# Kernel tuning notes

Measured on AMD Instinct MI355X. Metric: run time of the kernel, lower is better.

The kernel has to match this reference:

```python
import jax, jax.numpy as jnp
import numpy as np

HIDDEN_SIZE = 512  # H * d = 8 * 64


def setup_inputs() -> dict:
    key = jax.random.key(0)
    kq, kk, kv = jax.random.split(key, 3)
    B, H, S, d = 2, 8, 4096, 64
    Q = jax.random.normal(kq, (B, H, S, d), dtype=jnp.float32)
    K = jax.random.normal(kk, (B, H, d, S), dtype=jnp.float32)  # pre-transposed, as the torch module expects
    V = jax.random.normal(kv, (B, H, S, d), dtype=jnp.float32)
    return {"Q": Q, "K": K, "V": V}


def reference(Q, K, V):
    B, H, S, d = Q.shape
    scale = 1.0 / np.sqrt(HIDDEN_SIZE).astype(np.float32)
    # e: [B,H,S,S] -- full score matrix, as in the original
    e = jnp.einsum('bhsd,bhdt->bhst', Q, K) * scale
    # FAITHFUL quirk: nn.Softmax(dim=1) normalizes over the HEAD axis, not keys
    a = jax.nn.softmax(e, axis=1)
    o = jnp.einsum('bhst,bhtd->bhsd', a, V)
    # torch .view(B, S, hidden): raw contiguous reshape of [B,H,S,d]
    return o.reshape(B, S, HIDDEN_SIZE)
```

## Files before the change

kernel.cpp:

```cpp
#include <hip/hip_runtime.h>
#include <hip/hip_fp16.h>

#define S_LEN 4096
#define NHEAD 8
#define HEADD 64
#define BM 64
#define BN 32
#define TSPLIT 4
#define NTILE (S_LEN / (TSPLIT * BN))
#define O_ELEMS (2 * NHEAD * S_LEN * HEADD)
#define SCALE 0.04419417382415922f
#define EAPAD 36

#define KT_BYTES (2ull * NHEAD * S_LEN * HEADD * 2)
#define VT_OFF   KT_BYTES
#define PART_OFF (2 * KT_BYTES)
#define WS_FULL  (PART_OFF + (size_t)TSPLIT * O_ELEMS * 4)

typedef __attribute__((ext_vector_type(8))) short   short8;
typedef __attribute__((ext_vector_type(4))) float   float4v;
typedef __attribute__((ext_vector_type(4))) unsigned short ushort4v;

__device__ __forceinline__ unsigned short f2bf(float f) {
  unsigned int u = __float_as_uint(f);
  u += 0x7FFFu + ((u >> 16) & 1u);
  return (unsigned short)(u >> 16);
}

__global__ __launch_bounds__(256)
void prepass_cvt(const float* __restrict__ K, const float* __restrict__ V,
                 unsigned short* __restrict__ Kt, unsigned short* __restrict__ Vt) {
  __shared__ __align__(16) unsigned short lds[64][72];
  const int tid = threadIdx.x;
  const int isV = blockIdx.x >> 10;
  const int idx = blockIdx.x & 1023;
  const int bh  = idx >> 6;
  const int t0  = (idx & 63) << 6;
  if (!isV) {
    const float* in = K + (size_t)bh * HEADD * S_LEN;
#pragma unroll
    for (int j = 0; j < 16; ++j) {
      int li = j * 256 + tid;
      int k = li >> 6, t = li & 63;
      lds[t][k] = f2bf(in[(size_t)k * S_LEN + t0 + t]);
    }
    __syncthreads();
    unsigned short* out = Kt + (size_t)bh * S_LEN * HEADD;
    int t = tid >> 2, k0 = (tid & 3) << 4;
    *(short8*)(out + (size_t)(t0 + t) * HEADD + k0)     = *(const short8*)&lds[t][k0];
    *(short8*)(out + (size_t)(t0 + t) * HEADD + k0 + 8) = *(const short8*)&lds[t][k0 + 8];
  } else {
    const float* in = V + (size_t)bh * S_LEN * HEADD;
#pragma unroll
    for (int j = 0; j < 16; ++j) {
      int li = j * 256 + tid;
      int t = li >> 6, d = li & 63;
      lds[d][t] = f2bf(in[(size_t)(t0 + t) * HEADD + d]);
    }
    __syncthreads();
    unsigned short* out = Vt + (size_t)bh * HEADD * S_LEN;
    int d = tid >> 2, c0 = (tid & 3) << 4;
    *(short8*)(out + (size_t)d * S_LEN + t0 + c0)     = *(const short8*)&lds[d][c0];
    *(short8*)(out + (size_t)d * S_LEN + t0 + c0 + 8) = *(const short8*)&lds[d][c0 + 8];
  }
}

__global__ __launch_bounds__(512, 4)
void attn_main(const float* __restrict__ Q, const unsigned short* __restrict__ Kt,
               const unsigned short* __restrict__ Vt, float* __restrict__ outp,
               int atomic_mode) {
  __shared__ __align__(16) unsigned short EA[2][NHEAD][BM][EAPAD];

  const int tid  = threadIdx.x;
  const int h    = tid >> 6;
  const int lane = tid & 63;
  const int quad = lane >> 4;
  const int l15  = lane & 15;
  const int combo = blockIdx.x & 7;
  const int b  = combo >> 2;
  const int tc = combo & 3;
  const int s0 = (blockIdx.x >> 3) * BM;

  const float* Qg = Q + (size_t)(b * NHEAD + h) * S_LEN * HEADD;
  const unsigned short* Kth = Kt + (size_t)(b * NHEAD + h) * S_LEN * HEADD;
  const unsigned short* Vth = Vt + (size_t)(b * NHEAD + h) * HEADD * S_LEN;

  short8 qf[4][2];
#pragma unroll
  for (int ss = 0; ss < 4; ++ss)
#pragma unroll
    for (int kk = 0; kk < 2; ++kk) {
      const float* p = Qg + (size_t)(s0 + ss * 16 + l15) * HEADD + kk * 32 + quad * 8;
      float4v a0 = *(const float4v*)p;
      float4v a1 = *(const float4v*)(p + 4);
      short8 f;
      f[0] = (short)f2bf(a0[0]); f[1] = (short)f2bf(a0[1]);
      f[2] = (short)f2bf(a0[2]); f[3] = (short)f2bf(a0[3]);
      f[4] = (short)f2bf(a1[0]); f[5] = (short)f2bf(a1[1]);
      f[6] = (short)f2bf(a1[2]); f[7] = (short)f2bf(a1[3]);
      qf[ss][kk] = f;
    }

  float4v acc[4][4];
#pragma unroll
  for (int ss = 0; ss < 4; ++ss)
#pragma unroll
    for (int ds = 0; ds < 4; ++ds)
      acc[ss][ds] = (float4v){0.f, 0.f, 0.f, 0.f};

  const int s_sm = tid >> 3;
  const int t4   = (tid & 7) * 4;

  for (int it = 0; it < NTILE; ++it) {
    const int t0 = tc * (S_LEN / TSPLIT) + it * BN;
    const int p  = it & 1;

    short8 kf[2][2];
#pragma unroll
    for (int ts = 0; ts < 2; ++ts)
#pragma unroll
      for (int kk = 0; kk < 2; ++kk)
        kf[ts][kk] = *(const short8*)(Kth + (size_t)(t0 + ts * 16 + l15) * HEADD + kk * 32 + quad * 8);

#pragma unroll
    for (int ts = 0; ts < 2; ++ts)
#pragma unroll
      for (int ss = 0; ss < 4; ++ss) {
        float4v e = (float4v){0.f, 0.f, 0.f, 0.f};
        e = __builtin_amdgcn_mfma_f32_16x16x32_bf16(qf[ss][0], kf[ts][0], e, 0, 0, 0);
        e = __builtin_amdgcn_mfma_f32_16x16x32_bf16(qf[ss][1], kf[ts][1], e, 0, 0, 0);
#pragma unroll
        for (int r = 0; r < 4; ++r)
          EA[p][h][ss * 16 + quad * 4 + r][ts * 16 + l15] =
              __half_as_ushort(__float2half(e[r] * SCALE));
      }
    __syncthreads();

    {
      float ev[8][4];
#pragma unroll
      for (int hh = 0; hh < 8; ++hh) {
        ushort4v u = *(const ushort4v*)&EA[p][hh][s_sm][t4];
#pragma unroll
        for (int c = 0; c < 4; ++c) ev[hh][c] = __half2float(__ushort_as_half(u[c]));
      }
#pragma unroll
      for (int c = 0; c < 4; ++c) {
        float sum = 0.f;
#pragma unroll
        for (int hh = 0; hh < 8; ++hh) { float x = __expf(ev[hh][c]); ev[hh][c] = x; sum += x; }
        float inv = __builtin_amdgcn_rcpf(sum);
#pragma unroll
        for (int hh = 0; hh < 8; ++hh) ev[hh][c] *= inv;
      }
#pragma unroll
      for (int hh = 0; hh < 8; ++hh) {
        ushort4v u;
#pragma unroll
        for (int c = 0; c < 4; ++c) u[c] = f2bf(ev[hh][c]);
        *(ushort4v*)&EA[p][hh][s_sm][t4] = u;
      }
    }
    __syncthreads();

    short8 af[4], vf[4];
#pragma unroll
    for (int ss = 0; ss < 4; ++ss) {
      union { short8 s8; ushort4v u4[2]; } t;
      t.u4[0] = *(const ushort4v*)&EA[p][h][ss * 16 + l15][quad * 8];
      t.u4[1] = *(const ushort4v*)&EA[p][h][ss * 16 + l15][quad * 8 + 4];
      af[ss] = t.s8;
    }
#pragma unroll
    for (int ds = 0; ds < 4; ++ds)
      vf[ds] = *(const short8*)(Vth + (size_t)(ds * 16 + l15) * S_LEN + t0 + quad * 8);
#pragma unroll
    for (int ss = 0; ss < 4; ++ss)
#pragma unroll
      for (int ds = 0; ds < 4; ++ds)
        acc[ss][ds] = __builtin_amdgcn_mfma_f32_16x16x32_bf16(af[ss], vf[ds], acc[ss][ds], 0, 0, 0);
  }

  float* Og = outp + (atomic_mode ? (size_t)0 : (size_t)tc * O_ELEMS) +
              (size_t)(b * NHEAD + h) * S_LEN * HEADD;
#pragma unroll
  for (int ss = 0; ss < 4; ++ss)
#pragma unroll
    for (int ds = 0; ds < 4; ++ds)
#pragma unroll
      for (int r = 0; r < 4; ++r) {
        size_t off = (size_t)(s0 + ss * 16 + quad * 4 + r) * HEADD + ds * 16 + l15;
        if (atomic_mode) atomicAdd(&Og[off], acc[ss][ds][r]);
        else             Og[off] = acc[ss][ds][r];
      }
}

__global__ __launch_bounds__(256)
void reduce_partials(const float* __restrict__ part, float* __restrict__ out) {
  const int n4 = O_ELEMS / 4;
  const float4v* p = (const float4v*)part;
  float4v* o = (float4v*)out;
  for (int i = blockIdx.x * 256 + threadIdx.x; i < n4; i += gridDim.x * 256) {
    float4v v = p[i] + p[n4 + i] + p[2 * n4 + i] + p[3 * n4 + i];
    o[i] = v;
  }
}

__global__ __launch_bounds__(512, 2)
void attn_fallback(const float* __restrict__ Qg0, const float* __restrict__ Kg0,
                   const float* __restrict__ Vg0, float* __restrict__ Og0) {
  __shared__ __align__(16) unsigned short Klds[NHEAD][BN][72];
  __shared__ __align__(16) unsigned short Vlds[NHEAD][HEADD][40];
  __shared__ __align__(16) unsigned short EA2[NHEAD][BM][40];
  const int tid = threadIdx.x, h = tid >> 6, lane = tid & 63, quad = lane >> 4, l15 = lane & 15;
  const int b = blockIdx.x >> 6, s0 = (blockIdx.x & 63) * BM;
  const float* Qg = Qg0 + ((size_t)(b * NHEAD + h)) * S_LEN * HEADD;
  const float* Kg = Kg0 + ((size_t)(b * NHEAD + h)) * HEADD * S_LEN;
  const float* Vg = Vg0 + ((size_t)(b * NHEAD + h)) * S_LEN * HEADD;
  float* Og = Og0 + ((size_t)(b * NHEAD + h)) * S_LEN * HEADD;
  short8 qf[4][2];
#pragma unroll
  for (int ss = 0; ss < 4; ++ss)
#pragma unroll
    for (int kk = 0; kk < 2; ++kk) {
      const float* p = Qg + (size_t)(s0 + ss * 16 + l15) * HEADD + kk * 32 + quad * 8;
      float4v a0 = *(const float4v*)p; float4v a1 = *(const float4v*)(p + 4);
      short8 f;
      f[0] = (short)f2bf(a0[0]); f[1] = (short)f2bf(a0[1]); f[2] = (short)f2bf(a0[2]); f[3] = (short)f2bf(a0[3]);
      f[4] = (short)f2bf(a1[0]); f[5] = (short)f2bf(a1[1]); f[6] = (short)f2bf(a1[2]); f[7] = (short)f2bf(a1[3]);
      qf[ss][kk] = f;
    }
  float4v acc[4][4];
#pragma unroll
  for (int ss = 0; ss < 4; ++ss)
#pragma unroll
    for (int ds = 0; ds < 4; ++ds) acc[ss][ds] = (float4v){0.f, 0.f, 0.f, 0.f};
  const int koct = lane >> 3, kt4 = (lane & 7) * 4, vdq = lane & 15, vtg = lane >> 4;
  const int s_sm = tid >> 3, t4_sm = (tid & 7) * 4;
  for (int it = 0; it < S_LEN / BN; ++it) {
    const int t0 = it * BN;
    {
      float buf[8][4];
#pragma unroll
      for (int j = 0; j < 8; ++j) {
        float4v v = *(const float4v*)(Kg + (size_t)(koct * 8 + j) * S_LEN + t0 + kt4);
        buf[j][0] = v[0]; buf[j][1] = v[1]; buf[j][2] = v[2]; buf[j][3] = v[3];
      }
#pragma unroll
      for (int c = 0; c < 4; ++c) {
        short8 f;
#pragma unroll
        for (int j = 0; j < 8; ++j) f[j] = (short)f2bf(buf[j][c]);
        *(short8*)&Klds[h][kt4 + c][koct * 8] = f;
      }
    }
    {
      float buf[8][4];
#pragma unroll
      for (int j = 0; j < 8; ++j) {
        float4v v = *(const float4v*)(Vg + (size_t)(t0 + vtg * 8 + j) * HEADD + vdq * 4);
        buf[j][0] = v[0]; buf[j][1] = v[1]; buf[j][2] = v[2]; buf[j][3] = v[3];
      }
#pragma unroll
      for (int c = 0; c < 4; ++c) {
        short8 f;
#pragma unroll
        for (int j = 0; j < 8; ++j) f[j] = (short)f2bf(buf[j][c]);
        *(short8*)&Vlds[h][vdq * 4 + c][vtg * 8] = f;
      }
    }
    __syncthreads();
#pragma unroll
    for (int ts = 0; ts < 2; ++ts) {
      short8 kf0 = *(const short8*)&Klds[h][ts * 16 + l15][quad * 8];
      short8 kf1 = *(const short8*)&Klds[h][ts * 16 + l15][32 + quad * 8];
#pragma unroll
      for (int ss = 0; ss < 4; ++ss) {
        float4v e = (float4v){0.f, 0.f, 0.f, 0.f};
        e = __builtin_amdgcn_mfma_f32_16x16x32_bf16(qf[ss][0], kf0, e, 0, 0, 0);
        e = __builtin_amdgcn_mfma_f32_16x16x32_bf16(qf[ss][1], kf1, e, 0, 0, 0);
#pragma unroll
        for (int r = 0; r < 4; ++r)
          EA2[h][ss * 16 + quad * 4 + r][ts * 16 + l15] = __half_as_ushort(__float2half(e[r] * SCALE));
      }
    }
    __syncthreads();
    {
      float ev[8][4];
#pragma unroll
      for (int hh = 0; hh < 8; ++hh) {
        ushort4v u = *(const ushort4v*)&EA2[hh][s_sm][t4_sm];
#pragma unroll
        for (int c = 0; c < 4; ++c) ev[hh][c] = __half2float(__ushort_as_half(u[c]));
      }
#pragma unroll
      for (int c = 0; c < 4; ++c) {
        float m = ev[0][c];
#pragma unroll
        for (int hh = 1; hh < 8; ++hh) m = fmaxf(m, ev[hh][c]);
        float sum = 0.f;
#pragma unroll
        for (int hh = 0; hh < 8; ++hh) { float x = __expf(ev[hh][c] - m); ev[hh][c] = x; sum += x; }
        float inv = __builtin_amdgcn_rcpf(sum);
#pragma unroll
        for (int hh = 0; hh < 8; ++hh) ev[hh][c] *= inv;
      }
#pragma unroll
      for (int hh = 0; hh < 8; ++hh) {
        ushort4v u;
#pragma unroll
        for (int c = 0; c < 4; ++c) u[c] = f2bf(ev[hh][c]);
        *(ushort4v*)&EA2[hh][s_sm][t4_sm] = u;
      }
    }
    __syncthreads();
    {
      short8 af[4], vf[4];
#pragma unroll
      for (int ss = 0; ss < 4; ++ss) af[ss] = *(const short8*)&EA2[h][ss * 16 + l15][quad * 8];
#pragma unroll
      for (int ds = 0; ds < 4; ++ds) vf[ds] = *(const short8*)&Vlds[h][ds * 16 + l15][quad * 8];
#pragma unroll
      for (int ss = 0; ss < 4; ++ss)
#pragma unroll
        for (int ds = 0; ds < 4; ++ds)
          acc[ss][ds] = __builtin_amdgcn_mfma_f32_16x16x32_bf16(af[ss], vf[ds], acc[ss][ds], 0, 0, 0);
    }
    __syncthreads();
  }
#pragma unroll
  for (int ss = 0; ss < 4; ++ss)
#pragma unroll
    for (int ds = 0; ds < 4; ++ds)
#pragma unroll
      for (int r = 0; r < 4; ++r)
        Og[(size_t)(s0 + ss * 16 + quad * 4 + r) * HEADD + ds * 16 + l15] = acc[ss][ds][r];
}

extern "C" void kernel_launch(void* const* d_in, const int* in_sizes, int n_in,
                              void* d_out, int out_size, void* d_ws, size_t ws_size,
                              hipStream_t stream) {
  const float* Q = (const float*)d_in[0];
  const float* K = (const float*)d_in[1];
  const float* V = (const float*)d_in[2];
  float* O = (float*)d_out;

  if (ws_size >= WS_FULL) {
    unsigned short* Kt = (unsigned short*)d_ws;
    unsigned short* Vt = (unsigned short*)((char*)d_ws + VT_OFF);
    float* part = (float*)((char*)d_ws + PART_OFF);
    hipLaunchKernelGGL(prepass_cvt, dim3(2048), dim3(256), 0, stream, K, V, Kt, Vt);
    hipLaunchKernelGGL(attn_main, dim3(512), dim3(512), 0, stream, Q, Kt, Vt, part, 0);
    hipLaunchKernelGGL(reduce_partials, dim3(1024), dim3(256), 0, stream, part, O);
  } else if (ws_size >= PART_OFF) {
    unsigned short* Kt = (unsigned short*)d_ws;
    unsigned short* Vt = (unsigned short*)((char*)d_ws + VT_OFF);
    hipMemsetAsync(O, 0, (size_t)O_ELEMS * 4, stream);
    hipLaunchKernelGGL(prepass_cvt, dim3(2048), dim3(256), 0, stream, K, V, Kt, Vt);
    hipLaunchKernelGGL(attn_main, dim3(512), dim3(512), 0, stream, Q, Kt, Vt, O, 1);
  } else {
    hipLaunchKernelGGL(attn_fallback, dim3(128), dim3(512), 0, stream, Q, K, V, O);
  }
}
```

Measured before the change: 383.4 us.

## Split key axis eight ways with smaller row tiles and bf16-packed partials

Halves the query tile to 32 rows and doubles the key split to 8, so the main kernel launches 2048 blocks instead of 512 and occupancy is raised. The softmax scale and log2(e) are folded into K during the bf16 prepass, so the softmax uses a raw v_exp_f32 with no per-element scale. Partial outputs are packed as bf16 pairs to halve partial-buffer traffic, and the reduction kernel unpacks and sums eight partials. The atomic middle path is removed. The risks are precision loss from bf16 partials and the work duplicated across more splits.

After: 361.6 us. -5.7%, faster.

```diff
diff --git a/kernel.cpp b/kernel.cpp
--- a/kernel.cpp
+++ b/kernel.cpp
@@ -4,27 +4,30 @@
 #define S_LEN 4096
 #define NHEAD 8
 #define HEADD 64
-#define BM 64
+#define BM 32
 #define BN 32
-#define TSPLIT 4
-#define NTILE (S_LEN / (TSPLIT * BN))
-#define O_ELEMS (2 * NHEAD * S_LEN * HEADD)
-#define SCALE 0.04419417382415922f
-#define EAPAD 36
+#define TSPLIT 8
+#define TCHUNK (S_LEN / TSPLIT)
+#define NTILE (TCHUNK / BN)
+#define EAP 48
+#define KPRE 0.0637588696f
 
 #define KT_BYTES (2ull * NHEAD * S_LEN * HEADD * 2)
 #define VT_OFF   KT_BYTES
 #define PART_OFF (2 * KT_BYTES)
-#define WS_FULL  (PART_OFF + (size_t)TSPLIT * O_ELEMS * 4)
+#define PART_U32 (16ull * NHEAD * 2048 * 64)
+#define WS_FULL  (PART_OFF + PART_U32 * 4)
 
 typedef __attribute__((ext_vector_type(8))) short   short8;
 typedef __attribute__((ext_vector_type(4))) float   float4v;
-typedef __attribute__((ext_vector_type(4))) unsigned short ushort4v;
 
 __device__ __forceinline__ unsigned short f2bf(float f) {
   unsigned int u = __float_as_uint(f);
   u += 0x7FFFu + ((u >> 16) & 1u);
   return (unsigned short)(u >> 16);
+}
+__device__ __forceinline__ float fast_exp2(float x) {
+  float r; asm("v_exp_f32 %0, %1" : "=v"(r) : "v"(x)); return r;
 }
 
 __global__ __launch_bounds__(256)
@@ -42,7 +45,7 @@
     for (int j = 0; j < 16; ++j) {
       int li = j * 256 + tid;
       int k = li >> 6, t = li & 63;
-      lds[t][k] = f2bf(in[(size_t)k * S_LEN + t0 + t]);
+      lds[t][k] = f2bf(in[(size_t)k * S_LEN + t0 + t] * KPRE);
     }
     __syncthreads();
     unsigned short* out = Kt + (size_t)bh * S_LEN * HEADD;
@@ -65,29 +68,28 @@
   }
 }
 
-__global__ __launch_bounds__(512, 4)
+__global__ __launch_bounds__(512, 6)
 void attn_main(const float* __restrict__ Q, const unsigned short* __restrict__ Kt,
-               const unsigned short* __restrict__ Vt, float* __restrict__ outp,
-               int atomic_mode) {
-  __shared__ __align__(16) unsigned short EA[2][NHEAD][BM][EAPAD];
+               const unsigned short* __restrict__ Vt, unsigned int* __restrict__ part) {
+  __shared__ __align__(16) unsigned short EA[2][NHEAD][BM][EAP];
 
   const int tid  = threadIdx.x;
   const int h    = tid >> 6;
   const int lane = tid & 63;
   const int quad = lane >> 4;
   const int l15  = lane & 15;
-  const int combo = blockIdx.x & 7;
-  const int b  = combo >> 2;
-  const int tc = combo & 3;
-  const int s0 = (blockIdx.x >> 3) * BM;
+  const int combo = blockIdx.x & 15;
+  const int b  = combo & 1;
+  const int tc = combo >> 1;
+  const int s0 = (blockIdx.x >> 4) * BM;
 
   const float* Qg = Q + (size_t)(b * NHEAD + h) * S_LEN * HEADD;
   const unsigned short* Kth = Kt + (size_t)(b * NHEAD + h) * S_LEN * HEADD;
   const unsigned short* Vth = Vt + (size_t)(b * NHEAD + h) * HEADD * S_LEN;
 
-  short8 qf[4][2];
-#pragma unroll
-  for (int ss = 0; ss < 4; ++ss)
+  short8 qf[2][2];
+#pragma unroll
+  for (int ss = 0; ss < 2; ++ss)
 #pragma unroll
     for (int kk = 0; kk < 2; ++kk) {
       const float* p = Qg + (size_t)(s0 + ss * 16 + l15) * HEADD + kk * 32 + quad * 8;
@@ -101,123 +103,145 @@
       qf[ss][kk] = f;
     }
 
-  float4v acc[4][4];
-#pragma unroll
-  for (int ss = 0; ss < 4; ++ss)
-#pragma unroll
-    for (int ds = 0; ds < 4; ++ds)
-      acc[ss][ds] = (float4v){0.f, 0.f, 0.f, 0.f};
-
-  const int s_sm = tid >> 3;
-  const int t4   = (tid & 7) * 4;
-
-  for (int it = 0; it < NTILE; ++it) {
-    const int t0 = tc * (S_LEN / TSPLIT) + it * BN;
-    const int p  = it & 1;
-
-    short8 kf[2][2];
-#pragma unroll
-    for (int ts = 0; ts < 2; ++ts)
-#pragma unroll
-      for (int kk = 0; kk < 2; ++kk)
-        kf[ts][kk] = *(const short8*)(Kth + (size_t)(t0 + ts * 16 + l15) * HEADD + kk * 32 + quad * 8);
-
-#pragma unroll
-    for (int ts = 0; ts < 2; ++ts)
-#pragma unroll
-      for (int ss = 0; ss < 4; ++ss) {
-        float4v e = (float4v){0.f, 0.f, 0.f, 0.f};
-        e = __builtin_amdgcn_mfma_f32_16x16x32_bf16(qf[ss][0], kf[ts][0], e, 0, 0, 0);
-        e = __builtin_amdgcn_mfma_f32_16x16x32_bf16(qf[ss][1], kf[ts][1], e, 0, 0, 0);
-#pragma unroll
-        for (int r = 0; r < 4; ++r)
-          EA[p][h][ss * 16 + quad * 4 + r][ts * 16 + l15] =
-              __half_as_ushort(__float2half(e[r] * SCALE));
-      }
-    __syncthreads();
-
-    {
-      float ev[8][4];
-#pragma unroll
-      for (int hh = 0; hh < 8; ++hh) {
-        ushort4v u = *(const ushort4v*)&EA[p][hh][s_sm][t4];
-#pragma unroll
-        for (int c = 0; c < 4; ++c) ev[hh][c] = __half2float(__ushort_as_half(u[c]));
-      }
-#pragma unroll
-      for (int c = 0; c < 4; ++c) {
-        float sum = 0.f;
-#pragma unroll
-        for (int hh = 0; hh < 8; ++hh) { float x = __expf(ev[hh][c]); ev[hh][c] = x; sum += x; }
+  float4v acc[2][4];
+#pragma unroll
+  for (int ss = 0; ss < 2; ++ss)
+#pragma unroll
+    for (int df = 0; df < 4; ++df)
+      acc[ss][df] = (float4v){0.f, 0.f, 0.f, 0.f};
+
+  const int s_sm = tid >> 4;
+  const int tp   = tid & 15;
+
+  int t0 = tc * TCHUNK;
+  for (int it = 0; it < NTILE; ++it, t0 += BN) {
+    const int p = it & 1;
+
+    {
+      short8 kf[2][2];
+#pragma unroll
+      for (int ts = 0; ts < 2; ++ts)
+#pragma unroll
+        for (int kh = 0; kh < 2; ++kh)
+          kf[ts][kh] = *(const short8*)(Kth + (size_t)(t0 + ts * 16 + l15) * HEADD + kh * 32 + quad * 8);
+#pragma unroll
+      for (int ss = 0; ss < 2; ++ss)
+#pragma unroll
+        for (int ts = 0; ts < 2; ++ts) {
+          float4v e = (float4v){0.f, 0.f, 0.f, 0.f};
+          e = __builtin_amdgcn_mfma_f32_16x16x32_bf16(qf[ss][0], kf[ts][0], e, 0, 0, 0);
+          e = __builtin_amdgcn_mfma_f32_16x16x32_bf16(qf[ss][1], kf[ts][1], e, 0, 0, 0);
+#pragma unroll
+          for (int r = 0; r < 4; ++r)
+            EA[p][h][ss * 16 + quad * 4 + r][ts * 16 + l15] =
+                __half_as_ushort(__float2half(e[r]));
+        }
+    }
+    __syncthreads();
+
+    {
+      unsigned int x[8];
+#pragma unroll
+      for (int hh = 0; hh < 8; ++hh)
+        x[hh] = *(const unsigned int*)&EA[p][hh][s_sm][tp * 2];
+      {
+        float pe[8]; float sum = 0.f;
+#pragma unroll
+        for (int hh = 0; hh < 8; ++hh) {
+          pe[hh] = fast_exp2(__half2float(__ushort_as_half((unsigned short)(x[hh] & 0xffffu))));
+          sum += pe[hh];
+        }
         float inv = __builtin_amdgcn_rcpf(sum);
 #pragma unroll
-        for (int hh = 0; hh < 8; ++hh) ev[hh][c] *= inv;
-      }
-#pragma unroll
-      for (int hh = 0; hh < 8; ++hh) {
-        ushort4v u;
-#pragma unroll
-        for (int c = 0; c < 4; ++c) u[c] = f2bf(ev[hh][c]);
-        *(ushort4v*)&EA[p][hh][s_sm][t4] = u;
-      }
-    }
-    __syncthreads();
-
-    short8 af[4], vf[4];
-#pragma unroll
-    for (int ss = 0; ss < 4; ++ss) {
-      union { short8 s8; ushort4v u4[2]; } t;
-      t.u4[0] = *(const ushort4v*)&EA[p][h][ss * 16 + l15][quad * 8];
-      t.u4[1] = *(const ushort4v*)&EA[p][h][ss * 16 + l15][quad * 8 + 4];
-      af[ss] = t.s8;
-    }
-#pragma unroll
-    for (int ds = 0; ds < 4; ++ds)
-      vf[ds] = *(const short8*)(Vth + (size_t)(ds * 16 + l15) * S_LEN + t0 + quad * 8);
-#pragma unroll
-    for (int ss = 0; ss < 4; ++ss)
-#pragma unroll
-      for (int ds = 0; ds < 4; ++ds)
-        acc[ss][ds] = __builtin_amdgcn_mfma_f32_16x16x32_bf16(af[ss], vf[ds], acc[ss][ds], 0, 0, 0);
-  }
-
-  float* Og = outp + (atomic_mode ? (size_t)0 : (size_t)tc * O_ELEMS) +
-              (size_t)(b * NHEAD + h) * S_LEN * HEADD;
-#pragma unroll
-  for (int ss = 0; ss < 4; ++ss)
-#pragma unroll
-    for (int ds = 0; ds < 4; ++ds)
-#pragma unroll
-      for (int r = 0; r < 4; ++r) {
-        size_t off = (size_t)(s0 + ss * 16 + quad * 4 + r) * HEADD + ds * 16 + l15;
-        if (atomic_mode) atomicAdd(&Og[off], acc[ss][ds][r]);
-        else             Og[off] = acc[ss][ds][r];
+        for (int hh = 0; hh < 8; ++hh) {
+          unsigned int u = __float_as_uint(pe[hh] * inv) + 0x8000u;
+          EA[p][hh][s_sm][tp * 2] = (unsigned short)(u >> 16);
+        }
+      }
+      {
+        float pe[8]; float sum = 0.f;
+#pragma unroll
+        for (int hh = 0; hh < 8; ++hh) {
+          pe[hh] = fast_exp2(__half2float(__ushort_as_half((unsigned short)(x[hh] >> 16))));
+          sum += pe[hh];
+        }
+        float inv = __builtin_amdgcn_rcpf(sum);
+#pragma unroll
+        for (int hh = 0; hh < 8; ++hh) {
+          unsigned int u = __float_as_uint(pe[hh] * inv) + 0x8000u;
+          EA[p][hh][s_sm][tp * 2 + 1] = (unsigned short)(u >> 16);
+        }
+      }
+    }
+    __syncthreads();
+
+    {
+      short8 vf[4];
+#pragma unroll
+      for (int df = 0; df < 4; ++df)
+        vf[df] = *(const short8*)(Vth + (size_t)(df * 16 + l15) * S_LEN + t0 + quad * 8);
+      short8 af[2];
+#pragma unroll
+      for (int ss = 0; ss < 2; ++ss)
+        af[ss] = *(const short8*)&EA[p][h][ss * 16 + l15][quad * 8];
+#pragma unroll
+      for (int ss = 0; ss < 2; ++ss)
+#pragma unroll
+        for (int df = 0; df < 4; ++df)
+          acc[ss][df] = __builtin_amdgcn_mfma_f32_16x16x32_bf16(af[ss], vf[df], acc[ss][df], 0, 0, 0);
+    }
+  }
+
+  unsigned int* pb = part + ((size_t)(tc * 2 + b) * NHEAD + h) * (2048ull * 64);
+  const int spb = (s0 >> 1) + quad * 2;
+#pragma unroll
+  for (int ss = 0; ss < 2; ++ss)
+#pragma unroll
+    for (int df = 0; df < 4; ++df)
+#pragma unroll
+      for (int rp = 0; rp < 2; ++rp) {
+        unsigned int ulo = __float_as_uint(acc[ss][df][rp * 2])     + 0x8000u;
+        unsigned int uhi = __float_as_uint(acc[ss][df][rp * 2 + 1]) + 0x8000u;
+        unsigned int pk  = __builtin_amdgcn_perm(uhi, ulo, 0x07060302u);
+        pb[(size_t)(spb + ss * 8 + rp) * 64 + df * 16 + l15] = pk;
       }
 }
 
 __global__ __launch_bounds__(256)
-void reduce_partials(const float* __restrict__ part, float* __restrict__ out) {
-  const int n4 = O_ELEMS / 4;
-  const float4v* p = (const float4v*)part;
-  float4v* o = (float4v*)out;
-  for (int i = blockIdx.x * 256 + threadIdx.x; i < n4; i += gridDim.x * 256) {
-    float4v v = p[i] + p[n4 + i] + p[2 * n4 + i] + p[3 * n4 + i];
-    o[i] = v;
-  }
+void reduce_partials(const unsigned int* __restrict__ part, float* __restrict__ out) {
+  const size_t TCSTRIDE = 2097152;
+  size_t i = ((size_t)blockIdx.x * 256 + threadIdx.x) * 4;
+  if (i >= TCSTRIDE) return;
+  float lo[4] = {0.f, 0.f, 0.f, 0.f}, hi[4] = {0.f, 0.f, 0.f, 0.f};
+#pragma unroll
+  for (int tc = 0; tc < 8; ++tc) {
+    uint4 v = *(const uint4*)(part + tc * TCSTRIDE + i);
+    lo[0] += __uint_as_float(v.x << 16); hi[0] += __uint_as_float(v.x & 0xffff0000u);
+    lo[1] += __uint_as_float(v.y << 16); hi[1] += __uint_as_float(v.y & 0xffff0000u);
+    lo[2] += __uint_as_float(v.z << 16); hi[2] += __uint_as_float(v.z & 0xffff0000u);
+    lo[3] += __uint_as_float(v.w << 16); hi[3] += __uint_as_float(v.w & 0xffff0000u);
+  }
+  size_t bh = i >> 17;
+  unsigned int r = (unsigned int)(i & 131071u);
+  unsigned int sp = r >> 6, d = r & 63u;
+  float* o = out + ((size_t)bh * S_LEN + 2 * sp) * HEADD + d;
+  *(float4v*)o        = (float4v){lo[0], lo[1], lo[2], lo[3]};
+  *(float4v*)(o + 64) = (float4v){hi[0], hi[1], hi[2], hi[3]};
 }
 
 __global__ __launch_bounds__(512, 2)
 void attn_fallback(const float* __restrict__ Qg0, const float* __restrict__ Kg0,
                    const float* __restrict__ Vg0, float* __restrict__ Og0) {
-  __shared__ __align__(16) unsigned short Klds[NHEAD][BN][72];
+  __shared__ __align__(16) unsigned short Klds[NHEAD][32][72];
   __shared__ __align__(16) unsigned short Vlds[NHEAD][HEADD][40];
-  __shared__ __align__(16) unsigned short EA2[NHEAD][BM][40];
+  __shared__ __align__(16) unsigned short EA2[NHEAD][64][40];
   const int tid = threadIdx.x, h = tid >> 6, lane = tid & 63, quad = lane >> 4, l15 = lane & 15;
-  const int b = blockIdx.x >> 6, s0 = (blockIdx.x & 63) * BM;
+  const int b = blockIdx.x >> 6, s0 = (blockIdx.x & 63) * 64;
   const float* Qg = Qg0 + ((size_t)(b * NHEAD + h)) * S_LEN * HEADD;
   const float* Kg = Kg0 + ((size_t)(b * NHEAD + h)) * HEADD * S_LEN;
   const float* Vg = Vg0 + ((size_t)(b * NHEAD + h)) * S_LEN * HEADD;
   float* Og = Og0 + ((size_t)(b * NHEAD + h)) * S_LEN * HEADD;
+  const float SC = 0.04419417382415922f;
   short8 qf[4][2];
 #pragma unroll
   for (int ss = 0; ss < 4; ++ss)
@@ -237,8 +261,8 @@
     for (int ds = 0; ds < 4; ++ds) acc[ss][ds] = (float4v){0.f, 0.f, 0.f, 0.f};
   const int koct = lane >> 3, kt4 = (lane & 7) * 4, vdq = lane & 15, vtg = lane >> 4;
   const int s_sm = tid >> 3, t4_sm = (tid & 7) * 4;
-  for (int it = 0; it < S_LEN / BN; ++it) {
-    const int t0 = it * BN;
+  for (int it = 0; it < S_LEN / 32; ++it) {
+    const int t0 = it * 32;
     {
       float buf[8][4];
 #pragma unroll
@@ -281,7 +305,7 @@
         e = __builtin_amdgcn_mfma_f32_16x16x32_bf16(qf[ss][1], kf1, e, 0, 0, 0);
 #pragma unroll
         for (int r = 0; r < 4; ++r)
-          EA2[h][ss * 16 + quad * 4 + r][ts * 16 + l15] = __half_as_ushort(__float2half(e[r] * SCALE));
+          EA2[h][ss * 16 + quad * 4 + r][ts * 16 + l15] = __half_as_ushort(__float2half(e[r] * SC));
       }
     }
     __syncthreads();
@@ -289,9 +313,11 @@
       float ev[8][4];
 #pragma unroll
       for (int hh = 0; hh < 8; ++hh) {
-        ushort4v u = *(const ushort4v*)&EA2[hh][s_sm][t4_sm];
-#pragma unroll
-        for (int c = 0; c < 4; ++c) ev[hh][c] = __half2float(__ushort_as_half(u[c]));
+        unsigned long long u = *(const unsigned long long*)&EA2[hh][s_sm][t4_sm];
+        ev[hh][0] = __half2float(__ushort_as_half((unsigned short)u));
+        ev[hh][1] = __half2float(__ushort_as_half((unsigned short)(u >> 16)));
+        ev[hh][2] = __half2float(__ushort_as_half((unsigned short)(u >> 32)));
+        ev[hh][3] = __half2float(__ushort_as_half((unsigned short)(u >> 48)));
       }
 #pragma unroll
       for (int c = 0; c < 4; ++c) {
@@ -307,10 +333,10 @@
       }
 #pragma unroll
       for (int hh = 0; hh < 8; ++hh) {
-        ushort4v u;
-#pragma unroll
-        for (int c = 0; c < 4; ++c) u[c] = f2bf(ev[hh][c]);
-        *(ushort4v*)&EA2[hh][s_sm][t4_sm] = u;
+        unsigned short u0 = f2bf(ev[hh][0]), u1 = f2bf(ev[hh][1]), u2 = f2bf(ev[hh][2]), u3 = f2bf(ev[hh][3]);
+        unsigned long long w = (unsigned long long)u0 | ((unsigned long long)u1 << 16) |
+                               ((unsigned long long)u2 << 32) | ((unsigned long long)u3 << 48);
+        *(unsigned long long*)&EA2[hh][s_sm][t4_sm] = w;
       }
     }
     __syncthreads();
@@ -348,16 +374,10 @@
   if (ws_size >= WS_FULL) {
     unsigned short* Kt = (unsigned short*)d_ws;
     unsigned short* Vt = (unsigned short*)((char*)d_ws + VT_OFF);
-    float* part = (float*)((char*)d_ws + PART_OFF);
+    unsigned int* part = (unsigned int*)((char*)d_ws + PART_OFF);
     hipLaunchKernelGGL(prepass_cvt, dim3(2048), dim3(256), 0, stream, K, V, Kt, Vt);
-    hipLaunchKernelGGL(attn_main, dim3(512), dim3(512), 0, stream, Q, Kt, Vt, part, 0);
-    hipLaunchKernelGGL(reduce_partials, dim3(1024), dim3(256), 0, stream, part, O);
-  } else if (ws_size >= PART_OFF) {
-    unsigned short* Kt = (unsigned short*)d_ws;
-    unsigned short* Vt = (unsigned short*)((char*)d_ws + VT_OFF);
-    hipMemsetAsync(O, 0, (size_t)O_ELEMS * 4, stream);
-    hipLaunchKernelGGL(prepass_cvt, dim3(2048), dim3(256), 0, stream, K, V, Kt, Vt);
-    hipLaunchKernelGGL(attn_main, dim3(512), dim3(512), 0, stream, Q, Kt, Vt, O, 1);
+    hipLaunchKernelGGL(attn_main, dim3(2048), dim3(512), 0, stream, Q, Kt, Vt, part);
+    hipLaunchKernelGGL(reduce_partials, dim3(2048), dim3(256), 0, stream, part, O);
   } else {
     hipLaunchKernelGGL(attn_fallback, dim3(128), dim3(512), 0, stream, Q, K, V, O);
   }
```
